# Performance work log

Hardware: AMD Instinct MI355X
Metric: run time of the kernel (lower is better)

Reference implementation:

```python
import jax, jax.numpy as jnp
import numpy as np
from jax import lax

# Module hyperparameters (is_act=True, n_bits=4, granu=8)
N_BITS = 4
GRANU = 8
RANGE = 2 ** N_BITS - 1          # 15
L = GRANU * RANGE                # 120, flattened table length
NBINS = L + 1                    # histc bins = table_q.numel()//2 + 1


def setup_inputs() -> dict:
    key = jax.random.key(0)
    k1, k2, k3 = jax.random.split(key, 3)
    x = jax.random.normal(k1, (64, 256, 56, 56), dtype=jnp.float32)
    table = jax.random.normal(k2, (RANGE, GRANU), dtype=jnp.float32)
    scale = jax.random.uniform(k3, (1,), dtype=jnp.float32)  # nonzero -> skips lazy init branch
    tau = jnp.ones((1,), dtype=jnp.float32)
    return {"x": x, "table": table, "scale": scale, "tau": tau}


def _forward(x, table, scale, tau):
    # lazy scale init: if scale param == 0, set to log(3 * std(x)) (a .data assign -> stop_gradient)
    std_init = lax.stop_gradient(jnp.log(jnp.std(x, ddof=1) * 3.0))
    scale_p = jnp.where(scale[0] == 0.0, std_init, scale[0])
    sc = jnp.exp(scale_p)

    # ---- _gen_table (training): softmax over granu, then conv1d with the
    # step kernel T (ones on first L taps) == causal cumulative sum over the
    # flattened probabilities -> monotone CDF table.
    prob = jax.nn.softmax(table / tau[0], axis=1)          # [RANGE, GRANU]
    cdf = jnp.cumsum(prob.reshape(-1))                     # [L]
    # is_act: F.pad top by L+1 -> [zeros(L+1), cdf], length 2L+1; divide by range
    table_q = jnp.concatenate([jnp.zeros((L + 1,), dtype=cdf.dtype), cdf]) / RANGE  # [2L+1]

    # ---- _lookup (training, is_act)
    grid = jnp.clip(x / sc, -1.0, 1.0)
    gsd = lax.stop_gradient(grid)

    # torch.histc(grid.data, NBINS) with default min=max=0 -> bins over [min, max] of data
    hist, _ = jnp.histogram(gsd, bins=NBINS)               # [NBINS]
    wgt = jnp.sqrt(hist.astype(jnp.float32))
    wgt = jnp.concatenate([jnp.zeros((L,), dtype=jnp.float32), wgt]) + 1e-5  # pad top by L -> [2L+1]

    # gradient reweighting: value unchanged, grads scaled by numel/(nbins*wgt)
    tq_d = lax.stop_gradient(table_q)
    table_q = tq_d + (table_q - tq_d) / wgt * (x.size / NBINS)

    # nearest grid_sample with border padding == rounded integer gather
    s = L  # table_q.shape // 2
    idx = jnp.clip(jnp.round(gsd * s).astype(jnp.int32) + s, 0, 2 * s)
    x_q = table_q[idx]                                     # gather, shape of x

    # straight-through: grads flow through grid into x and scale
    x_q = (x_q + grid - gsd) * sc
    return x_q


def reference(x, table, scale, tau):
    return _forward(x, table, scale, tau)
```

## Files before the change

### kernel.cpp

```cpp
#include <hip/hip_runtime.h>
#include <math.h>

#define RANGE 15
#define GRANU 8
#define LTAB 120
#define TQ (2 * LTAB + 1)


__global__ __launch_bounds__(256) void prep_kernel(const float* __restrict__ table,
                                                   const float* __restrict__ tau,
                                                   float* __restrict__ wsf,
                                                   double* __restrict__ wsd) {
    __shared__ float prob[LTAB];
    const int t = threadIdx.x;
    if (t < 2) wsd[t] = 0.0;
    const float tauv = tau[0];
    if (t < RANGE) {
        float y[GRANU];
        float m = -INFINITY;
        #pragma unroll
        for (int c = 0; c < GRANU; ++c) {
            y[c] = table[t * GRANU + c] / tauv;
            m = fmaxf(m, y[c]);
        }
        float e[GRANU];
        float s = 0.0f;
        #pragma unroll
        for (int c = 0; c < GRANU; ++c) {
            e[c] = expf(y[c] - m);
            s += e[c];
        }
        #pragma unroll
        for (int c = 0; c < GRANU; ++c) prob[t * GRANU + c] = e[c] / s;
    }
    __syncthreads();
    if (t == 0) {
        for (int j = 0; j <= LTAB; ++j) wsf[1 + j] = 0.0f;
        float acc = 0.0f;
        for (int j = 0; j < LTAB; ++j) {
            acc += prob[j];
            wsf[1 + (LTAB + 1) + j] = acc / 15.0f;
        }
    }
}

__global__ __launch_bounds__(256) void std_reduce_kernel(const float* __restrict__ x,
                                                         const float* __restrict__ scale,
                                                         double* __restrict__ wsd,
                                                         int n) {
    if (scale[0] != 0.0f) return;
    double s = 0.0, s2 = 0.0;
    const int stride = gridDim.x * blockDim.x;
    for (int i = blockIdx.x * blockDim.x + threadIdx.x; i < n; i += stride) {
        double v = (double)x[i];
        s += v;
        s2 += v * v;
    }
    #pragma unroll
    for (int off = 32; off > 0; off >>= 1) {
        s  += __shfl_down(s, off);
        s2 += __shfl_down(s2, off);
    }
    if ((threadIdx.x & 63) == 0) {
        atomicAdd(&wsd[0], s);
        atomicAdd(&wsd[1], s2);
    }
}

__global__ void finalize_sc_kernel(const float* __restrict__ scale,
                                   const double* __restrict__ wsd,
                                   float* __restrict__ wsf,
                                   int n) {
    if (threadIdx.x == 0 && blockIdx.x == 0) {
        const float sp = scale[0];
        float sc;
        if (sp != 0.0f) {
            sc = expf(sp);
        } else {
            double sum = wsd[0], sumsq = wsd[1];
            double mean = sum / (double)n;
            double var = (sumsq - sum * mean) / (double)(n - 1);
            float stdf = (float)sqrt(var);
            sc = expf(logf(stdf * 3.0f));
        }
        wsf[0] = sc;
    }
}

__device__ __forceinline__ float lcq_one(float xv, float sc, const float* __restrict__ tq) {
    float g = xv / sc;
    g = fminf(fmaxf(g, -1.0f), 1.0f);
    int idx = (int)rintf(g * 120.0f) + 120;
    idx = min(max(idx, 0), 240);
    return ((tq[idx] + g) - g) * sc;
}

__global__ __launch_bounds__(256) void lookup_kernel(const float4* __restrict__ x4,
                                                     float4* __restrict__ out4,
                                                     const float* __restrict__ x,
                                                     float* __restrict__ out,
                                                     const float* __restrict__ wsf,
                                                     int n4, int n) {
    __shared__ float tq[TQ];
    __shared__ float s_sc;
    for (int i = threadIdx.x; i < TQ; i += 256) tq[i] = wsf[1 + i];
    if (threadIdx.x == 0) s_sc = wsf[0];
    __syncthreads();
    const float sc = s_sc;

    const int gid = blockIdx.x * 256 + threadIdx.x;
    const int stride = gridDim.x * 256;
    for (int i = gid; i < n4; i += stride) {
        float4 v = x4[i];
        float4 o;
        o.x = lcq_one(v.x, sc, tq);
        o.y = lcq_one(v.y, sc, tq);
        o.z = lcq_one(v.z, sc, tq);
        o.w = lcq_one(v.w, sc, tq);
        out4[i] = o;
    }
    for (int i = n4 * 4 + gid; i < n; i += stride) {
        out[i] = lcq_one(x[i], sc, tq);
    }
}

extern "C" void kernel_launch(void* const* d_in, const int* in_sizes, int n_in,
                              void* d_out, int out_size, void* d_ws, size_t ws_size,
                              hipStream_t stream) {
    const float* x     = (const float*)d_in[0];
    const float* table = (const float*)d_in[1];
    const float* scale = (const float*)d_in[2];
    const float* tau   = (const float*)d_in[3];
    float* out = (float*)d_out;

    float*  wsf = (float*)d_ws;
    double* wsd = (double*)((char*)d_ws + 1024);

    const int n  = in_sizes[0];
    const int n4 = n / 4;

    hipLaunchKernelGGL(prep_kernel, dim3(1), dim3(256), 0, stream, table, tau, wsf, wsd);
    hipLaunchKernelGGL(std_reduce_kernel, dim3(512), dim3(256), 0, stream, x, scale, wsd, n);
    hipLaunchKernelGGL(finalize_sc_kernel, dim3(1), dim3(64), 0, stream, scale, wsd, wsf, n);
    hipLaunchKernelGGL(lookup_kernel, dim3(2048), dim3(256), 0, stream,
                       (const float4*)x, (float4*)out, x, out, wsf, n4, n);
}
```

Baseline: 352.9 us.

## Merge prep/std/finalize kernels, use per-block partials, nontemporal 2x-unrolled lookup

```diff
diff --git a/kernel.cpp b/kernel.cpp
--- a/kernel.cpp
+++ b/kernel.cpp
@@ -5,85 +5,74 @@
 #define GRANU 8
 #define LTAB 120
 #define TQ (2 * LTAB + 1)
+#define NPART 512
+
+typedef float floatx4 __attribute__((ext_vector_type(4)));
 
 
-__global__ __launch_bounds__(256) void prep_kernel(const float* __restrict__ table,
-                                                   const float* __restrict__ tau,
-                                                   float* __restrict__ wsf,
-                                                   double* __restrict__ wsd) {
-    __shared__ float prob[LTAB];
+__global__ __launch_bounds__(256) void prep_std_kernel(const float* __restrict__ table,
+                                                       const float* __restrict__ tau,
+                                                       const float* __restrict__ x,
+                                                       const float* __restrict__ scale,
+                                                       float* __restrict__ wsf,
+                                                       double* __restrict__ wsd,
+                                                       int n) {
     const int t = threadIdx.x;
-    if (t < 2) wsd[t] = 0.0;
-    const float tauv = tau[0];
-    if (t < RANGE) {
-        float y[GRANU];
-        float m = -INFINITY;
-        #pragma unroll
-        for (int c = 0; c < GRANU; ++c) {
-            y[c] = table[t * GRANU + c] / tauv;
-            m = fmaxf(m, y[c]);
+    if (blockIdx.x == 0) {
+        __shared__ float prob[LTAB];
+        const float tauv = tau[0];
+        if (t < RANGE) {
+            float y[GRANU];
+            float m = -INFINITY;
+            #pragma unroll
+            for (int c = 0; c < GRANU; ++c) {
+                y[c] = table[t * GRANU + c] / tauv;
+                m = fmaxf(m, y[c]);
+            }
+            float e[GRANU];
+            float s = 0.0f;
+            #pragma unroll
+            for (int c = 0; c < GRANU; ++c) {
+                e[c] = expf(y[c] - m);
+                s += e[c];
+            }
+            #pragma unroll
+            for (int c = 0; c < GRANU; ++c) prob[t * GRANU + c] = e[c] / s;
         }
-        float e[GRANU];
-        float s = 0.0f;
-        #pragma unroll
-        for (int c = 0; c < GRANU; ++c) {
-            e[c] = expf(y[c] - m);
-            s += e[c];
+        __syncthreads();
+        if (t == 0) {
+            for (int j = 0; j <= LTAB; ++j) wsf[j] = 0.0f;
+            float acc = 0.0f;
+            for (int j = 0; j < LTAB; ++j) {
+                acc += prob[j];
+                wsf[(LTAB + 1) + j] = acc / 15.0f;
+            }
         }
-        #pragma unroll
-        for (int c = 0; c < GRANU; ++c) prob[t * GRANU + c] = e[c] / s;
+        return;
     }
-    __syncthreads();
-    if (t == 0) {
-        for (int j = 0; j <= LTAB; ++j) wsf[1 + j] = 0.0f;
-        float acc = 0.0f;
-        for (int j = 0; j < LTAB; ++j) {
-            acc += prob[j];
-            wsf[1 + (LTAB + 1) + j] = acc / 15.0f;
-        }
+    const int b = blockIdx.x - 1;
+    if (scale[0] != 0.0f) {
+        if (t == 0) { wsd[2 * b] = 0.0; wsd[2 * b + 1] = 0.0; }
+        return;
     }
-}
-
-__global__ __launch_bounds__(256) void std_reduce_kernel(const float* __restrict__ x,
-                                                         const float* __restrict__ scale,
-                                                         double* __restrict__ wsd,
-                                                         int n) {
-    if (scale[0] != 0.0f) return;
     double s = 0.0, s2 = 0.0;
-    const int stride = gridDim.x * blockDim.x;
-    for (int i = blockIdx.x * blockDim.x + threadIdx.x; i < n; i += stride) {
+    const int stride = NPART * 256;
+    for (int i = b * 256 + t; i < n; i += stride) {
         double v = (double)x[i];
         s += v;
         s2 += v * v;
     }
+    __shared__ double red[2][4];
     #pragma unroll
     for (int off = 32; off > 0; off >>= 1) {
         s  += __shfl_down(s, off);
         s2 += __shfl_down(s2, off);
     }
-    if ((threadIdx.x & 63) == 0) {
-        atomicAdd(&wsd[0], s);
-        atomicAdd(&wsd[1], s2);
-    }
-}
-
-__global__ void finalize_sc_kernel(const float* __restrict__ scale,
-                                   const double* __restrict__ wsd,
-                                   float* __restrict__ wsf,
-                                   int n) {
-    if (threadIdx.x == 0 && blockIdx.x == 0) {
-        const float sp = scale[0];
-        float sc;
-        if (sp != 0.0f) {
-            sc = expf(sp);
-        } else {
-            double sum = wsd[0], sumsq = wsd[1];
-            double mean = sum / (double)n;
-            double var = (sumsq - sum * mean) / (double)(n - 1);
-            float stdf = (float)sqrt(var);
-            sc = expf(logf(stdf * 3.0f));
-        }
-        wsf[0] = sc;
+    if ((t & 63) == 0) { red[0][t >> 6] = s; red[1][t >> 6] = s2; }
+    __syncthreads();
+    if (t == 0) {
+        wsd[2 * b]     = red[0][0] + red[0][1] + red[0][2] + red[0][3];
+        wsd[2 * b + 1] = red[1][0] + red[1][1] + red[1][2] + red[1][3];
     }
 }
 
@@ -95,32 +84,56 @@
     return ((tq[idx] + g) - g) * sc;
 }
 
-__global__ __launch_bounds__(256) void lookup_kernel(const float4* __restrict__ x4,
-                                                     float4* __restrict__ out4,
+__global__ __launch_bounds__(256) void lookup_kernel(const floatx4* __restrict__ x4,
+                                                     floatx4* __restrict__ out4,
                                                      const float* __restrict__ x,
                                                      float* __restrict__ out,
+                                                     const float* __restrict__ scale,
                                                      const float* __restrict__ wsf,
+                                                     const double* __restrict__ wsd,
                                                      int n4, int n) {
     __shared__ float tq[TQ];
     __shared__ float s_sc;
-    for (int i = threadIdx.x; i < TQ; i += 256) tq[i] = wsf[1 + i];
-    if (threadIdx.x == 0) s_sc = wsf[0];
+    for (int i = threadIdx.x; i < TQ; i += 256) tq[i] = wsf[i];
+    if (threadIdx.x == 0) {
+        const float sp = scale[0];
+        float sc;
+        if (sp != 0.0f) {
+            sc = expf(sp);
+        } else {
+            double sum = 0.0, sumsq = 0.0;
+            for (int b = 0; b < NPART; ++b) { sum += wsd[2 * b]; sumsq += wsd[2 * b + 1]; }
+            double mean = sum / (double)n;
+            double var = (sumsq - sum * mean) / (double)(n - 1);
+            sc = expf(logf((float)sqrt(var) * 3.0f));
+        }
+        s_sc = sc;
+    }
     __syncthreads();
     const float sc = s_sc;
 
-    const int gid = blockIdx.x * 256 + threadIdx.x;
+    int i = blockIdx.x * 256 + threadIdx.x;
     const int stride = gridDim.x * 256;
-    for (int i = gid; i < n4; i += stride) {
-        float4 v = x4[i];
-        float4 o;
-        o.x = lcq_one(v.x, sc, tq);
-        o.y = lcq_one(v.y, sc, tq);
-        o.z = lcq_one(v.z, sc, tq);
-        o.w = lcq_one(v.w, sc, tq);
-        out4[i] = o;
+    for (; i + stride < n4; i += 2 * stride) {
+        floatx4 a = __builtin_nontemporal_load(&x4[i]);
+        floatx4 b = __builtin_nontemporal_load(&x4[i + stride]);
+        floatx4 oa, ob;
+        oa.x = lcq_one(a.x, sc, tq); oa.y = lcq_one(a.y, sc, tq);
+        oa.z = lcq_one(a.z, sc, tq); oa.w = lcq_one(a.w, sc, tq);
+        ob.x = lcq_one(b.x, sc, tq); ob.y = lcq_one(b.y, sc, tq);
+        ob.z = lcq_one(b.z, sc, tq); ob.w = lcq_one(b.w, sc, tq);
+        __builtin_nontemporal_store(oa, &out4[i]);
+        __builtin_nontemporal_store(ob, &out4[i + stride]);
     }
-    for (int i = n4 * 4 + gid; i < n; i += stride) {
-        out[i] = lcq_one(x[i], sc, tq);
+    for (; i < n4; i += stride) {
+        floatx4 a = __builtin_nontemporal_load(&x4[i]);
+        floatx4 oa;
+        oa.x = lcq_one(a.x, sc, tq); oa.y = lcq_one(a.y, sc, tq);
+        oa.z = lcq_one(a.z, sc, tq); oa.w = lcq_one(a.w, sc, tq);
+        __builtin_nontemporal_store(oa, &out4[i]);
+    }
+    for (int j = n4 * 4 + blockIdx.x * 256 + threadIdx.x; j < n; j += stride) {
+        out[j] = lcq_one(x[j], sc, tq);
     }
 }
 
@@ -134,14 +147,13 @@
     float* out = (float*)d_out;
 
     float*  wsf = (float*)d_ws;
-    double* wsd = (double*)((char*)d_ws + 1024);
+    double* wsd = (double*)((char*)d_ws + 4096);
 
     const int n  = in_sizes[0];
     const int n4 = n / 4;
 
-    hipLaunchKernelGGL(prep_kernel, dim3(1), dim3(256), 0, stream, table, tau, wsf, wsd);
-    hipLaunchKernelGGL(std_reduce_kernel, dim3(512), dim3(256), 0, stream, x, scale, wsd, n);
-    hipLaunchKernelGGL(finalize_sc_kernel, dim3(1), dim3(64), 0, stream, scale, wsd, wsf, n);
+    hipLaunchKernelGGL(prep_std_kernel, dim3(NPART + 1), dim3(256), 0, stream,
+                       table, tau, x, scale, wsf, wsd, n);
     hipLaunchKernelGGL(lookup_kernel, dim3(2048), dim3(256), 0, stream,
-                       (const float4*)x, (float4*)out, x, out, wsf, n4, n);
+                       (const floatx4*)x, (floatx4*)out, x, out, scale, wsf, wsd, n4, n);
 }
```

Result: faster. 345.3 us (-2.2%).
